# Optimization experiments

Hardware: AMD Instinct MI355X
Metric: run time of the kernel (lower is better)

The kernel has to match this reference:

```python
import jax, jax.numpy as jnp
import numpy as np

B, C1, C2, H, W = 8, 256, 256, 64, 64
C = 256            # int(c1*e)
G = C // 16        # 16 groups (dg)
Cg = C // G        # 16 channels per group
K = 9              # 3x3 kernel sample points
BN_EPS = 1e-5

# kernel grid offsets for 3x3, dilation 1 (pad=1 centers the grid)
KH = jnp.array([-1, -1, -1, 0, 0, 0, 1, 1, 1], jnp.float32)
KW = jnp.array([-1, 0, 1, -1, 0, 1, -1, 0, 1], jnp.float32)


def setup_inputs() -> dict:
    key = jax.random.key(0)
    ks = jax.random.split(key, 10)
    x = jax.random.normal(ks[0], (B, C1, H, W), jnp.float32)
    w_cv1 = jax.random.normal(ks[1], (C, C1), jnp.float32) / np.sqrt(C1)
    b_cv1 = jax.random.normal(ks[2], (C,), jnp.float32) * 0.1
    # offset/mask linear (DCNv4 inits to zero; small scale keeps sampling sane)
    w_off = jax.random.normal(ks[3], (G * 3 * K, C), jnp.float32) * 0.01
    b_off = jax.random.normal(ks[4], (G * 3 * K,), jnp.float32) * 0.01
    w_cv2 = jax.random.normal(ks[5], (C2, C), jnp.float32) / np.sqrt(C)
    bn_gamma = jax.random.uniform(ks[6], (C2,), jnp.float32, 0.5, 1.5)
    bn_beta = jax.random.normal(ks[7], (C2,), jnp.float32) * 0.1
    bn_mean = jax.random.normal(ks[8], (C2,), jnp.float32) * 0.1
    bn_var = jax.random.uniform(ks[9], (C2,), jnp.float32, 0.5, 1.5)
    return dict(x=x, w_cv1=w_cv1, b_cv1=b_cv1, w_off=w_off, b_off=b_off,
                w_cv2=w_cv2, bn_gamma=bn_gamma, bn_beta=bn_beta,
                bn_mean=bn_mean, bn_var=bn_var)


def _gather(vflat, hi, wi):
    # vflat: (B, H*W, G, Cg); hi/wi: (B,H,W,K,G) float corner indices
    ok = ((hi >= 0) & (hi < H) & (wi >= 0) & (wi < W)).astype(vflat.dtype)
    idx = (jnp.clip(hi, 0, H - 1) * W + jnp.clip(wi, 0, W - 1)).astype(jnp.int32)
    idx = idx.reshape(B, H * W * K, G)
    idxb = jnp.broadcast_to(idx[..., None], (B, H * W * K, G, Cg))
    g = jnp.take_along_axis(vflat, idxb, axis=1)  # (B, HWK, G, Cg)
    return g.reshape(B, H, W, K, G, Cg), ok


def _dcnv4(v, off, mask):
    # v: (B,H,W,G,Cg); off: (B,H,W,G,K,2) (dh,dw); mask: (B,H,W,G,K)
    ii = jnp.arange(H, dtype=jnp.float32)
    jj = jnp.arange(W, dtype=jnp.float32)
    ph = ii[None, :, None, None, None] + KH[None, None, None, None, :] + off[..., 0]
    pw = jj[None, None, :, None, None] + KW[None, None, None, None, :] + off[..., 1]
    ph = ph.transpose(0, 1, 2, 4, 3)  # (B,H,W,K,G)
    pw = pw.transpose(0, 1, 2, 4, 3)
    h0 = jnp.floor(ph); w0 = jnp.floor(pw)
    ah = ph - h0; aw = pw - w0
    vflat = v.reshape(B, H * W, G, Cg)
    g00, ok00 = _gather(vflat, h0, w0)
    g01, ok01 = _gather(vflat, h0, w0 + 1)
    g10, ok10 = _gather(vflat, h0 + 1, w0)
    g11, ok11 = _gather(vflat, h0 + 1, w0 + 1)
    w00 = ((1 - ah) * (1 - aw) * ok00)[..., None]
    w01 = ((1 - ah) * aw * ok01)[..., None]
    w10 = (ah * (1 - aw) * ok10)[..., None]
    w11 = (ah * aw * ok11)[..., None]
    sample = w00 * g00 + w01 * g01 + w10 * g10 + w11 * g11  # (B,H,W,K,G,Cg)
    out = jnp.einsum('bhwkgc,bhwgk->bhwgc', sample, mask)
    return out.reshape(B, H, W, C).transpose(0, 3, 1, 2)  # NCHW


def reference(x, w_cv1, b_cv1, w_off, b_off, w_cv2, bn_gamma, bn_beta, bn_mean, bn_var):
    # cv1: 1x1 conv
    h1 = jnp.einsum('bchw,oc->bohw', x, w_cv1) + b_cv1[None, :, None, None]
    # offset/mask 1x1 projection, per-group layout [2K offsets, K masks]
    om = jnp.einsum('bchw,oc->bhwo', h1, w_off) + b_off
    om = om.reshape(B, H, W, G, 3 * K)
    off = om[..., :2 * K].reshape(B, H, W, G, K, 2)
    mask = om[..., 2 * K:]  # DCNv4: no softmax, used directly
    v = h1.transpose(0, 2, 3, 1).reshape(B, H, W, G, Cg)
    y = _dcnv4(v, off, mask)
    # cv2: 1x1 conv (no bias)
    y = jnp.einsum('bchw,oc->bohw', y, w_cv2)
    # BatchNorm (eval mode)
    scale = (bn_gamma / jnp.sqrt(bn_var + BN_EPS))[None, :, None, None]
    y = (y - bn_mean[None, :, None, None]) * scale + bn_beta[None, :, None, None]
    # SiLU
    return y * jax.nn.sigmoid(y)
```

## Files before the change

### kernel.cpp

```cpp
#include <hip/hip_runtime.h>

#define HW 4096
#define CCH 256
#define MOFF 432
#define PTOT 32768
#define PDIM 68
#define PIMG (PDIM*PDIM)

typedef unsigned short u16;
typedef __attribute__((ext_vector_type(8))) short short8;
typedef __attribute__((ext_vector_type(8))) unsigned short u16x8;
typedef __attribute__((ext_vector_type(4))) unsigned short u16x4;
typedef __attribute__((ext_vector_type(4))) float f32x4;

__device__ __forceinline__ u16 f2b(float f){
  unsigned int u = __float_as_uint(f);
  unsigned int rounding = 0x7FFFu + ((u >> 16) & 1u);
  return (u16)((u + rounding) >> 16);
}
__device__ __forceinline__ float b2f(u16 s){
  return __uint_as_float(((unsigned int)s) << 16);
}

__global__ __launch_bounds__(256) void k_prepw(
    const float* __restrict__ w1, const float* __restrict__ w2,
    const float* __restrict__ woff, const float* __restrict__ b1,
    const float* __restrict__ boff,
    const float* __restrict__ gamma, const float* __restrict__ beta,
    const float* __restrict__ mean, const float* __restrict__ var,
    u16* __restrict__ wb_big, u16* __restrict__ wb2,
    float* __restrict__ bnA, float* __restrict__ bnB,
    float* __restrict__ bcomb, u16* __restrict__ h1p){
  __shared__ float sbuf[512];
  int r = blockIdx.x, t = threadIdx.x;
  if (r < 256) wb_big[r*256 + t] = f2b(w1[r*256 + t]);
  else if (r < 336){ wb_big[(688 + (r - 256)) * 256 + t] = 0; }
  else if (r < 592){ int o = r - 336; wb2[o*256 + t] = f2b(w2[o*256 + t]); }
  else if (r == 592){
    if (t < 256){
      float sc = gamma[t] * rsqrtf(var[t] + 1e-5f);
      bnA[t] = sc;
      bnB[t] = beta[t] - mean[t] * sc;
    }
  } else if (r < 1121){
    int n = (r - 593) * 128 + (t >> 1);
    int seg = t & 1;
    int plane = n / 528, m = n % 528;
    int row, col;
    if (m < 136){ row = m / 68; col = m % 68; }
    else if (m < 272){ int mm = m - 136; row = 66 + mm / 68; col = mm % 68; }
    else { int mm = m - 272; row = 2 + (mm >> 2); int c4 = mm & 3; col = (c4 & 1) + 66 * (c4 >> 1); }
    u16x8 z = {};
    *reinterpret_cast<u16x8*>(&h1p[((size_t)plane * PIMG + row * PDIM + col) * 16 + seg * 8]) = z;
  } else {
    float* wr_ = sbuf;
    float* pb  = sbuf + 256;
    const int j = r - 1121;
    wr_[t] = woff[j * 256 + t];
    __syncthreads();
    float s = 0.f;
    #pragma unroll 8
    for (int m = 0; m < 256; ++m) s += wr_[m] * w1[m * 256 + t];
    wb_big[(256 + j) * 256 + t] = f2b(s);
    pb[t] = wr_[t] * b1[t];
    __syncthreads();
    if (t == 0){
      float bs = boff[j];
      for (int m = 0; m < 256; ++m) bs += pb[m];
      bcomb[j] = bs;
    }
  }
}

__global__ __launch_bounds__(256, 4) void k_mega(const float* __restrict__ x,
    const u16* __restrict__ Bw, const float* __restrict__ b1,
    const float* __restrict__ bcomb, u16* __restrict__ h1p,
    u16* __restrict__ om){
  __shared__ __align__(16) u16 A_lds[32 * 260];
  __shared__ __align__(16) u16 scr[128 * 72];

  const int stripe = blockIdx.x;
  const int tm = stripe * 32;
  const int b = tm >> 12, ploc = tm & 4095;
  const int t = threadIdx.x;
  const int lane = t & 63;
  const int w = t >> 6;

  {
    const float* xs = x + (size_t)b * 256 * HW + ploc;
    #pragma unroll
    for (int it = 0; it < 8; ++it){
      int idx = it * 256 + t;
      int c = idx >> 3;
      int p4 = (idx & 7) * 4;
      float4 v = *reinterpret_cast<const float4*>(&xs[(size_t)c * HW + p4]);
      A_lds[(p4 + 0) * 260 + c] = f2b(v.x);
      A_lds[(p4 + 1) * 260 + c] = f2b(v.y);
      A_lds[(p4 + 2) * 260 + c] = f2b(v.z);
      A_lds[(p4 + 3) * 260 + c] = f2b(v.w);
    }
  }
  __syncthreads();

  for (int oc6 = 0; oc6 < 6; ++oc6){
    const int tn = oc6 * 128;
    f32x4 acc[2][2] = {};

    for (int kc = 0; kc < 256; kc += 64){
      #pragma unroll
      for (int i = 0; i < 4; ++i){
        int idx = t + i * 256;
        int row = idx >> 3, cq = idx & 7;
        *reinterpret_cast<u16x8*>(&scr[row * 72 + cq * 8]) =
          *reinterpret_cast<const u16x8*>(&Bw[(size_t)(tn + row) * 256 + kc + cq * 8]);
      }
      __syncthreads();
      #pragma unroll
      for (int kk = 0; kk < 2; ++kk){
        short8 af[2], bf[2];
        #pragma unroll
        for (int m = 0; m < 2; ++m)
          af[m] = *reinterpret_cast<const short8*>(
            &A_lds[(m * 16 + (lane & 15)) * 260 + kc + kk * 32 + (lane >> 4) * 8]);
        #pragma unroll
        for (int n = 0; n < 2; ++n)
          bf[n] = *reinterpret_cast<const short8*>(
            &scr[(w * 32 + n * 16 + (lane & 15)) * 72 + kk * 32 + (lane >> 4) * 8]);
        #pragma unroll
        for (int m = 0; m < 2; ++m)
          #pragma unroll
          for (int n = 0; n < 2; ++n)
            acc[m][n] = __builtin_amdgcn_mfma_f32_16x16x32_bf16(af[m], bf[n], acc[m][n], 0, 0, 0);
      }
      __syncthreads();
    }

    constexpr int CP = 136;
    u16* C_l = scr;
    #pragma unroll
    for (int n = 0; n < 2; ++n){
      int col = w * 32 + n * 16 + (lane & 15);
      int o = tn + col;
      float bi = (o < 256) ? b1[o] : ((o - 256 < MOFF) ? bcomb[o - 256] : 0.f);
      #pragma unroll
      for (int m = 0; m < 2; ++m){
        int r0 = m * 16 + ((lane >> 4) << 2);
        #pragma unroll
        for (int j = 0; j < 4; ++j)
          C_l[(r0 + j) * CP + col] = f2b(acc[m][n][j] + bi);
      }
    }
    __syncthreads();
    #pragma unroll
    for (int pass = 0; pass < 2; ++pass){
      int row = pass * 16 + (t >> 4);
      int sg = t & 15;
      int oc = tn + sg * 8;
      int p = tm + row;
      if (tn < 256){
        int bb = p >> 12, ii = (p >> 6) & 63, jj = p & 63;
        size_t dst = ((size_t)(bb * 16 + (oc >> 4)) * PIMG + (ii + 2) * PDIM + jj + 2) * 16 + (oc & 15);
        *reinterpret_cast<u16x8*>(&h1p[dst]) =
          *reinterpret_cast<const u16x8*>(&C_l[row * CP + sg * 8]);
      } else {
        int occ = oc - 256;
        if (occ + 8 <= MOFF)
          *reinterpret_cast<u16x8*>(&om[(size_t)p * MOFF + occ]) =
            *reinterpret_cast<const u16x8*>(&C_l[row * CP + sg * 8]);
      }
    }
    __syncthreads();
  }
}

__global__ __launch_bounds__(256, 4) void k_sample(const u16* __restrict__ h1p,
    const u16* __restrict__ om, u16* __restrict__ ydcn){
  __shared__ float oms[4 * MOFF];
  __shared__ float recs[5 * 576];
  const int t = threadIdx.x;
  const int bid = blockIdx.x;
  const int img = bid & 7;
  const int loc = bid >> 3;
  const int pblk = img * 4096 + loc * 4;
  if (t < 216){
    u16x8 v = *reinterpret_cast<const u16x8*>(&om[(size_t)pblk * MOFF + t * 8]);
    float4 lo, hi;
    lo.x = b2f(v[0]); lo.y = b2f(v[1]); lo.z = b2f(v[2]); lo.w = b2f(v[3]);
    hi.x = b2f(v[4]); hi.y = b2f(v[5]); hi.z = b2f(v[6]); hi.w = b2f(v[7]);
    *reinterpret_cast<float4*>(&oms[t * 8]) = lo;
    *reinterpret_cast<float4*>(&oms[t * 8 + 4]) = hi;
  }
  __syncthreads();

  #pragma unroll
  for (int i = 0; i < 3; ++i){
    int r = t + i * 256;
    if (i < 2 || r < 576){
      int px = r / 144, rm = r % 144;
      int g = rm / 9, k = rm % 9;
      const float* ob = &oms[px * MOFF + g * 27];
      float oh = ob[2 * k], ow = ob[2 * k + 1], m = ob[18 + k];
      int hw = (pblk + px) & 4095;
      float ph = (float)((hw >> 6) + k / 3 - 1) + oh;
      float pw = (float)((hw & 63) + k % 3 - 1) + ow;
      float h0f = floorf(ph), w0f = floorf(pw);
      float ah = ph - h0f, aw = pw - w0f;
      int h0 = (int)h0f, w0 = (int)w0f;
      int hc = min(max(h0, -2), 64) + 2;
      int wc = min(max(w0, -2), 64) + 2;
      float mh1 = m * ah, mh0 = m - mh1;
      float c01 = mh0 * aw, c00 = mh0 - c01;
      float c11 = mh1 * aw, c10 = mh1 - c11;
      recs[r]            = c00;
      recs[576 + r]      = c01;
      recs[1152 + r]     = c10;
      recs[1728 + r]     = c11;
      recs[2304 + r]     = __uint_as_float((unsigned)((hc * PDIM + wc) << 5));
    }
  }
  __syncthreads();

  const int px = t >> 6;
  const int g = (t >> 2) & 15;
  const int q = t & 3;
  const int p = pblk + px;
  const int xsel = q >> 1;
  const u16* lanebase = h1p + (size_t)(img * 16 + g) * PIMG * 16 + q * 8;
  const int ri = px * 144 + g * 9;
  const float* ctp = &recs[xsel * 576 + ri];
  const float* cbp = &recs[1152 + xsel * 576 + ri];
  const float* adp = &recs[2304 + ri];

  float acc[8] = {};
  #pragma unroll
  for (int k = 0; k < 9; ++k){
    float ct = ctp[k];
    float cb = cbp[k];
    unsigned off = __float_as_uint(adp[k]);
    const u16* c0 = (const u16*)((const char*)lanebase + off);
    u16x8 tv = *reinterpret_cast<const u16x8*>(c0);
    u16x8 bv = *reinterpret_cast<const u16x8*>(c0 + PDIM * 16);
    #pragma unroll
    for (int j = 0; j < 8; ++j)
      acc[j] += ct * b2f(tv[j]) + cb * b2f(bv[j]);
  }
  #pragma unroll
  for (int j = 0; j < 8; ++j)
    acc[j] += __shfl_xor(acc[j], 2, 64);
  if (q < 2){
    u16x8 o8;
    #pragma unroll
    for (int j = 0; j < 8; ++j) o8[j] = f2b(acc[j]);
    *reinterpret_cast<u16x8*>(&ydcn[(size_t)p * 256 + g * 16 + q * 8]) = o8;
  }
}

__global__ __launch_bounds__(256) void k_gemm2(const u16* __restrict__ A,
    const u16* __restrict__ Bw, const float* __restrict__ bnA,
    const float* __restrict__ bnB, float* __restrict__ out){
  __shared__ __align__(16) u16 smem[(128 + 128) * 40];
  const int t = threadIdx.x;
  const int tm = blockIdx.x * 128;
  const int tn = blockIdx.y * 128;
  const int lane = t & 63;
  const int wid = t >> 6;
  const int wr = wid >> 1, wc = wid & 1;
  constexpr int BOFF = 128 * 40;

  f32x4 acc[4][4] = {};

  for (int kc = 0; kc < 256; kc += 32){
    #pragma unroll
    for (int i = 0; i < 2; ++i){
      int v = t + i * 256;
      int row = v >> 2, cq = v & 3;
      *reinterpret_cast<u16x8*>(&smem[row * 40 + cq * 8]) =
        *reinterpret_cast<const u16x8*>(&A[(size_t)(tm + row) * 256 + kc + cq * 8]);
    }
    #pragma unroll
    for (int i = 0; i < 2; ++i){
      int v = t + i * 256;
      int row = v >> 2, cq = v & 3;
      *reinterpret_cast<u16x8*>(&smem[BOFF + row * 40 + cq * 8]) =
        *reinterpret_cast<const u16x8*>(&Bw[(size_t)(tn + row) * 256 + kc + cq * 8]);
    }
    __syncthreads();
    short8 af[4], bf[4];
    #pragma unroll
    for (int m = 0; m < 4; ++m)
      af[m] = *reinterpret_cast<const short8*>(
        &smem[(wr * 64 + m * 16 + (lane & 15)) * 40 + (lane >> 4) * 8]);
    #pragma unroll
    for (int n = 0; n < 4; ++n)
      bf[n] = *reinterpret_cast<const short8*>(
        &smem[BOFF + (wc * 64 + n * 16 + (lane & 15)) * 40 + (lane >> 4) * 8]);
    #pragma unroll
    for (int m = 0; m < 4; ++m)
      #pragma unroll
      for (int n = 0; n < 4; ++n)
        acc[m][n] = __builtin_amdgcn_mfma_f32_16x16x32_bf16(af[m], bf[n], acc[m][n], 0, 0, 0);
    __syncthreads();
  }

  const int bimg = tm >> 12;
  const int ploc = tm & 4095;
  #pragma unroll
  for (int n = 0; n < 4; ++n){
    int o = tn + wc * 64 + n * 16 + (lane & 15);
    float sA = bnA[o], sB = bnB[o];
    #pragma unroll
    for (int m = 0; m < 4; ++m){
      int prow = wr * 64 + m * 16 + ((lane >> 4) << 2);
      f32x4 st;
      #pragma unroll
      for (int j = 0; j < 4; ++j){
        float y = acc[m][n][j] * sA + sB;
        st[j] = y / (1.f + expf(-y));
      }
      *reinterpret_cast<f32x4*>(&out[((size_t)(bimg * 256 + o)) * HW + ploc + prow]) = st;
    }
  }
}

extern "C" void kernel_launch(void* const* d_in, const int* in_sizes, int n_in,
                              void* d_out, int out_size, void* d_ws, size_t ws_size,
                              hipStream_t stream) {
  const float* x     = (const float*)d_in[0];
  const float* w1    = (const float*)d_in[1];
  const float* b1    = (const float*)d_in[2];
  const float* woff  = (const float*)d_in[3];
  const float* boff  = (const float*)d_in[4];
  const float* w2    = (const float*)d_in[5];
  const float* gamma = (const float*)d_in[6];
  const float* beta  = (const float*)d_in[7];
  const float* mean  = (const float*)d_in[8];
  const float* var   = (const float*)d_in[9];
  float* out = (float*)d_out;
  (void)in_sizes; (void)n_in; (void)out_size; (void)ws_size;

  u16* h1p    = (u16*)d_ws;
  u16* om     = h1p + (size_t)128 * PIMG * 16;
  u16* ydcn   = om + (size_t)PTOT * MOFF;
  u16* wb_big = ydcn + (size_t)PTOT * CCH;
  u16* wb2    = wb_big + 768 * 256;
  float* bnA  = (float*)(wb2 + 256 * 256);
  float* bnB  = bnA + 256;
  float* bcomb = bnB + 256;

  dim3 blk(256);
  k_prepw<<<dim3(1553), blk, 0, stream>>>(w1, w2, woff, b1, boff,
                                          gamma, beta, mean, var,
                                          wb_big, wb2, bnA, bnB, bcomb, h1p);
  k_mega<<<dim3(1024), blk, 0, stream>>>(x, wb_big, b1, bcomb, h1p, om);
  k_sample<<<dim3(PTOT / 4), blk, 0, stream>>>(h1p, om, ydcn);
  k_gemm2<<<dim3(PTOT / 128, 2), blk, 0, stream>>>(ydcn, wb2, bnA, bnB, out);
}
```

Before: 101.4 us.

## Keep activation fragments in registers and stream weights directly from global in k_mega

The first GEMM kernel is restructured so each block covers 64 pixels, with each wave holding its 16-pixel A fragments for the full K=256 in registers, loaded through a small transposing LDS tile. Weight fragments are read straight from global (L2-cached) memory per MFMA instead of being staged through shared LDS with block-wide barriers, and outputs are written through a per-wave LDS scratch using only wave barriers. The output channel loop now runs over 11 chunks of 64 (704 columns) instead of 6 of 128 (768), trimming padding work. This removes block-level synchronisation and LDS staging of weights, at the cost of more global/L2 weight traffic, higher register pressure (occupancy hint lowered to 2), and half as many blocks.

```diff
diff --git a/kernel.cpp b/kernel.cpp
--- a/kernel.cpp
+++ b/kernel.cpp
@@ -72,104 +72,85 @@
   }
 }
 
-__global__ __launch_bounds__(256, 4) void k_mega(const float* __restrict__ x,
+__global__ __launch_bounds__(256, 2) void k_mega(const float* __restrict__ x,
     const u16* __restrict__ Bw, const float* __restrict__ b1,
     const float* __restrict__ bcomb, u16* __restrict__ h1p,
     u16* __restrict__ om){
-  __shared__ __align__(16) u16 A_lds[32 * 260];
-  __shared__ __align__(16) u16 scr[128 * 72];
-
-  const int stripe = blockIdx.x;
-  const int tm = stripe * 32;
+  __shared__ __align__(16) u16 T_lds[64 * 72];
+  __shared__ __align__(16) u16 C_lds[4][16 * 72];
+
+  const int t = threadIdx.x;
+  const int tm = blockIdx.x * 64;
   const int b = tm >> 12, ploc = tm & 4095;
-  const int t = threadIdx.x;
   const int lane = t & 63;
   const int w = t >> 6;
-
-  {
-    const float* xs = x + (size_t)b * 256 * HW + ploc;
-    #pragma unroll
-    for (int it = 0; it < 8; ++it){
-      int idx = it * 256 + t;
-      int c = idx >> 3;
-      int p4 = (idx & 7) * 4;
-      float4 v = *reinterpret_cast<const float4*>(&xs[(size_t)c * HW + p4]);
-      A_lds[(p4 + 0) * 260 + c] = f2b(v.x);
-      A_lds[(p4 + 1) * 260 + c] = f2b(v.y);
-      A_lds[(p4 + 2) * 260 + c] = f2b(v.z);
-      A_lds[(p4 + 3) * 260 + c] = f2b(v.w);
-    }
-  }
-  __syncthreads();
-
-  for (int oc6 = 0; oc6 < 6; ++oc6){
-    const int tn = oc6 * 128;
-    f32x4 acc[2][2] = {};
-
-    for (int kc = 0; kc < 256; kc += 64){
+  const int lr = lane & 15, ls = lane >> 4;
+
+  short8 A[8];
+  const float* xs = x + (size_t)b * 256 * HW + ploc;
+  #pragma unroll
+  for (int rnd = 0; rnd < 4; ++rnd){
+    const int kc64 = rnd * 64;
+    #pragma unroll
+    for (int i = 0; i < 4; ++i){
+      int flat = t + i * 256;
+      int c_l = flat >> 4, seg = flat & 15;
+      float4 v = *reinterpret_cast<const float4*>(&xs[(size_t)(kc64 + c_l) * HW + seg * 4]);
+      T_lds[(seg * 4 + 0) * 72 + c_l] = f2b(v.x);
+      T_lds[(seg * 4 + 1) * 72 + c_l] = f2b(v.y);
+      T_lds[(seg * 4 + 2) * 72 + c_l] = f2b(v.z);
+      T_lds[(seg * 4 + 3) * 72 + c_l] = f2b(v.w);
+    }
+    __syncthreads();
+    #pragma unroll
+    for (int kk = 0; kk < 2; ++kk)
+      A[rnd * 2 + kk] = *reinterpret_cast<const short8*>(
+        &T_lds[(w * 16 + lr) * 72 + kk * 32 + ls * 8]);
+    __syncthreads();
+  }
+
+  const u16* bp = Bw + (size_t)lr * 256 + ls * 8;
+  u16* Cw = &C_lds[w][0];
+  const int pxw = tm + w * 16;
+
+  for (int oc = 0; oc < 11; ++oc){
+    const int o0 = oc * 64;
+    const u16* bpo = bp + (size_t)o0 * 256;
+    f32x4 acc[4] = {};
+    #pragma unroll
+    for (int kf = 0; kf < 8; ++kf){
       #pragma unroll
-      for (int i = 0; i < 4; ++i){
-        int idx = t + i * 256;
-        int row = idx >> 3, cq = idx & 7;
-        *reinterpret_cast<u16x8*>(&scr[row * 72 + cq * 8]) =
-          *reinterpret_cast<const u16x8*>(&Bw[(size_t)(tn + row) * 256 + kc + cq * 8]);
+      for (int nf = 0; nf < 4; ++nf){
+        short8 bf = *reinterpret_cast<const short8*>(bpo + nf * 4096 + kf * 32);
+        acc[nf] = __builtin_amdgcn_mfma_f32_16x16x32_bf16(A[kf], bf, acc[nf], 0, 0, 0);
       }
-      __syncthreads();
+    }
+    __builtin_amdgcn_wave_barrier();
+    #pragma unroll
+    for (int nf = 0; nf < 4; ++nf){
+      int o = o0 + nf * 16 + lr;
+      float bi = (o < 256) ? b1[o] : ((o < 688) ? bcomb[o - 256] : 0.f);
       #pragma unroll
-      for (int kk = 0; kk < 2; ++kk){
-        short8 af[2], bf[2];
-        #pragma unroll
-        for (int m = 0; m < 2; ++m)
-          af[m] = *reinterpret_cast<const short8*>(
-            &A_lds[(m * 16 + (lane & 15)) * 260 + kc + kk * 32 + (lane >> 4) * 8]);
-        #pragma unroll
-        for (int n = 0; n < 2; ++n)
-          bf[n] = *reinterpret_cast<const short8*>(
-            &scr[(w * 32 + n * 16 + (lane & 15)) * 72 + kk * 32 + (lane >> 4) * 8]);
-        #pragma unroll
-        for (int m = 0; m < 2; ++m)
-          #pragma unroll
-          for (int n = 0; n < 2; ++n)
-            acc[m][n] = __builtin_amdgcn_mfma_f32_16x16x32_bf16(af[m], bf[n], acc[m][n], 0, 0, 0);
+      for (int j = 0; j < 4; ++j)
+        Cw[(ls * 4 + j) * 72 + nf * 16 + lr] = f2b(acc[nf][j] + bi);
+    }
+    __builtin_amdgcn_wave_barrier();
+    #pragma unroll
+    for (int s = 0; s < 2; ++s){
+      int flat = lane + s * 64;
+      int row = flat >> 3, seg = flat & 7;
+      u16x8 v = *reinterpret_cast<const u16x8*>(&Cw[row * 72 + seg * 8]);
+      int px = pxw + row;
+      int o = o0 + seg * 8;
+      if (o < 256){
+        int ii = (px >> 6) & 63, jj = px & 63;
+        size_t dst = ((size_t)(b * 16 + (o >> 4)) * PIMG + (ii + 2) * PDIM + jj + 2) * 16 + (o & 15);
+        *reinterpret_cast<u16x8*>(&h1p[dst]) = v;
+      } else if (o < 688){
+        *reinterpret_cast<u16x8*>(&om[(size_t)px * MOFF + (o - 256)]) = v;
       }
-      __syncthreads();
-    }
-
-    constexpr int CP = 136;
-    u16* C_l = scr;
-    #pragma unroll
-    for (int n = 0; n < 2; ++n){
-      int col = w * 32 + n * 16 + (lane & 15);
-      int o = tn + col;
-      float bi = (o < 256) ? b1[o] : ((o - 256 < MOFF) ? bcomb[o - 256] : 0.f);
-      #pragma unroll
-      for (int m = 0; m < 2; ++m){
-        int r0 = m * 16 + ((lane >> 4) << 2);
-        #pragma unroll
-        for (int j = 0; j < 4; ++j)
-          C_l[(r0 + j) * CP + col] = f2b(acc[m][n][j] + bi);
-      }
-    }
-    __syncthreads();
-    #pragma unroll
-    for (int pass = 0; pass < 2; ++pass){
-      int row = pass * 16 + (t >> 4);
-      int sg = t & 15;
-      int oc = tn + sg * 8;
-      int p = tm + row;
-      if (tn < 256){
-        int bb = p >> 12, ii = (p >> 6) & 63, jj = p & 63;
-        size_t dst = ((size_t)(bb * 16 + (oc >> 4)) * PIMG + (ii + 2) * PDIM + jj + 2) * 16 + (oc & 15);
-        *reinterpret_cast<u16x8*>(&h1p[dst]) =
-          *reinterpret_cast<const u16x8*>(&C_l[row * CP + sg * 8]);
-      } else {
-        int occ = oc - 256;
-        if (occ + 8 <= MOFF)
-          *reinterpret_cast<u16x8*>(&om[(size_t)p * MOFF + occ]) =
-            *reinterpret_cast<const u16x8*>(&C_l[row * CP + sg * 8]);
-      }
-    }
-    __syncthreads();
+    }
+    __builtin_amdgcn_wave_barrier();
   }
 }
 
@@ -351,7 +332,7 @@
   k_prepw<<<dim3(1553), blk, 0, stream>>>(w1, w2, woff, b1, boff,
                                           gamma, beta, mean, var,
                                           wb_big, wb2, bnA, bnB, bcomb, h1p);
-  k_mega<<<dim3(1024), blk, 0, stream>>>(x, wb_big, b1, bcomb, h1p, om);
+  k_mega<<<dim3(512), blk, 0, stream>>>(x, wb_big, b1, bcomb, h1p, om);
   k_sample<<<dim3(PTOT / 4), blk, 0, stream>>>(h1p, om, ydcn);
   k_gemm2<<<dim3(PTOT / 128, 2), blk, 0, stream>>>(ydcn, wb2, bnA, bnB, out);
 }
```

Measured after the change: 154.1 us. +51.9%, slower.
